# Optimization experiments

Hardware: AMD Instinct MI355X
Metric: run time of the kernel (lower is better)

## Reference

```python
import jax, jax.numpy as jnp
import numpy as np

N_HEAD = 16
LN_EPS = 1e-5     # torch LayerNorm default
ATTN_EPS = 1e-6   # fast-transformers CausalLinearAttention eps


def layer_norm(x, g, b):
    mu = x.mean(-1, keepdims=True)
    var = ((x - mu) ** 2).mean(-1, keepdims=True)
    return (x - mu) * jax.lax.rsqrt(var + LN_EPS) * g + b


def favor(x, omega):
    # Favor/Performer softmax-kernel features.
    # x: [B,S,H,dh], omega: [dh, m/2] -> phi: [B,S,H,m] with m = 2*(dh//2) = dh
    dh = x.shape[-1]
    m = 2 * omega.shape[-1]
    xs = x * (dh ** -0.25)  # x * sqrt(softmax_temp), softmax_temp = 1/sqrt(dh)
    u = jnp.einsum('bshd,dm->bshm', xs, omega)
    h = 0.5 * jnp.sum(xs * xs, axis=-1, keepdims=True)  # ||x||^2 / 2
    return jnp.concatenate([jnp.exp(u - h), jnp.exp(-u - h)], axis=-1) * (m ** -0.5)


def causal_linear_attention(q, k, v):
    # q,k: [B,S,H,M] feature-mapped; v: [B,S,H,Dv]
    # out[i] = (phiQ_i @ sum_{j<=i} phiK_j v_j^T) / (phiQ_i . sum_{j<=i} phiK_j)
    B, S, H, M = q.shape
    Dv = v.shape[-1]
    qT = jnp.moveaxis(q, 1, 0)  # [S,B,H,M]
    kT = jnp.moveaxis(k, 1, 0)
    vT = jnp.moveaxis(v, 1, 0)  # [S,B,H,Dv]
    S0 = jnp.zeros((B, H, M, Dv), q.dtype)
    z0 = jnp.zeros((B, H, M), q.dtype)

    def step(carry, qkv):
        Sst, zst = carry
        qi, ki, vi = qkv
        Sst = Sst + ki[..., :, None] * vi[..., None, :]  # [B,H,M,Dv]
        zst = zst + ki                                   # [B,H,M]
        num = jnp.einsum('bhm,bhmd->bhd', qi, Sst)
        den = jnp.einsum('bhm,bhm->bh', qi, zst) + ATTN_EPS
        return (Sst, zst), num / den[..., None]

    _, out = jax.lax.scan(step, (S0, z0), (qT, kT, vT))
    return jnp.moveaxis(out, 0, 1)  # [B,S,H,Dv]


def forward(x, Wq, bq, Wk, bk, Wv, bv, Wo, bo, omega,
            ln1_g, ln1_b, ln2_g, ln2_b, W1, bf1, W2, bf2):
    L = Wq.shape[0]
    B, S, D = x.shape
    dh = D // N_HEAD
    out = x
    for l in range(L):  # fixed small layer count
        q = (out @ Wq[l] + bq[l]).reshape(B, S, N_HEAD, dh)
        k = (out @ Wk[l] + bk[l]).reshape(B, S, N_HEAD, dh)
        v = (out @ Wv[l] + bv[l]).reshape(B, S, N_HEAD, dh)
        Qf = favor(q, omega[l])
        Kf = favor(k, omega[l])
        a = causal_linear_attention(Qf, Kf, v).reshape(B, S, D)
        a = a @ Wo[l] + bo[l]
        h = layer_norm(out + a, ln1_g[l], ln1_b[l])          # norm1 (post-norm)
        y = jax.nn.relu(h @ W1[l] + bf1[l]) @ W2[l] + bf2[l]  # FFN
        out = layer_norm(h + y, ln2_g[l], ln2_b[l])          # norm2
    return out


def setup_inputs() -> dict:
    key = jax.random.key(0)
    L, B, S, D, DFF = 3, 2, 1024, 1024, 4096
    dh = D // N_HEAD
    ks = jax.random.split(key, 8)
    g = lambda k, shape: jax.random.normal(k, shape, jnp.float32) * 0.02
    return {
        'x': jax.random.normal(ks[0], (B, S, D), jnp.float32),
        'Wq': g(ks[1], (L, D, D)), 'bq': jnp.zeros((L, D), jnp.float32),
        'Wk': g(ks[2], (L, D, D)), 'bk': jnp.zeros((L, D), jnp.float32),
        'Wv': g(ks[3], (L, D, D)), 'bv': jnp.zeros((L, D), jnp.float32),
        'Wo': g(ks[4], (L, D, D)), 'bo': jnp.zeros((L, D), jnp.float32),
        'omega': jax.random.normal(ks[5], (L, dh, dh // 2), jnp.float32),
        'ln1_g': jnp.ones((L, D), jnp.float32), 'ln1_b': jnp.zeros((L, D), jnp.float32),
        'ln2_g': jnp.ones((L, D), jnp.float32), 'ln2_b': jnp.zeros((L, D), jnp.float32),
        'W1': g(ks[6], (L, D, DFF)), 'bf1': jnp.zeros((L, DFF), jnp.float32),
        'W2': g(ks[7], (L, DFF, D)), 'bf2': jnp.zeros((L, D), jnp.float32),
    }


def reference(x, Wq, bq, Wk, bk, Wv, bv, Wo, bo, omega,
              ln1_g, ln1_b, ln2_g, ln2_b, W1, bf1, W2, bf2):
    return forward(x, Wq, bq, Wk, bk, Wv, bv, Wo, bo, omega,
                   ln1_g, ln1_b, ln2_g, ln2_b, W1, bf1, W2, bf2)
```

## Files before the change

### kernel.cpp

```cpp
#include <hip/hip_runtime.h>

typedef unsigned int u32;
typedef unsigned short u16;
typedef unsigned long long u64;

#define LN_EPS 1e-5f
#define ATTN_EPS 1e-6f

typedef __bf16 bf16x8 __attribute__((ext_vector_type(8)));
typedef short shortx8 __attribute__((ext_vector_type(8)));
typedef float fx4 __attribute__((ext_vector_type(4)));
typedef float fx16 __attribute__((ext_vector_type(16)));

__device__ __forceinline__ u16 f2bf(float f){
  union{float f; u32 u;} x; x.f = f;
  u32 r = 0x7fffu + ((x.u>>16)&1u);
  return (u16)((x.u + r)>>16);
}
__device__ __forceinline__ float bf2f(u16 u){
  union{u32 u; float f;} x; x.u = ((u32)u)<<16; return x.f;
}
__device__ __forceinline__ bf16x8 ldfrag(const u16* p){
  return __builtin_bit_cast(bf16x8, *(const shortx8*)p);
}

__device__ __forceinline__ void async16(const void* g, void* l){
  typedef const __attribute__((address_space(1))) void gas_t;
  typedef __attribute__((address_space(3))) void las_t;
  __builtin_amdgcn_global_load_lds((gas_t*)(u64)g, (las_t*)(u32)(u64)l, 16, 0, 0);
}

__global__ void detect_kernel(const u16* __restrict__ ln1g, int* __restrict__ flag){
  if (threadIdx.x == 0 && blockIdx.x == 0)
    *flag = (ln1g[0] == 0x3F80u) ? 1 : 0;
}

__global__ __launch_bounds__(256) void cvt_small(
    const void* p0, const void* p1, const void* p2, const void* p3,
    const void* p4, const void* p5, const void* p6, const void* p7,
    const void* p8, const void* p9, const void* p10,
    float* __restrict__ out, const int* __restrict__ flagp)
{
  int i = blockIdx.x*256 + threadIdx.x;
  if (i >= 46080) return;
  const void* src; int off;
  if      (i < 3072)  { src=p0;  off=i; }
  else if (i < 6144)  { src=p1;  off=i-3072; }
  else if (i < 9216)  { src=p2;  off=i-6144; }
  else if (i < 12288) { src=p3;  off=i-9216; }
  else if (i < 18432) { src=p4;  off=i-12288; }
  else if (i < 21504) { src=p5;  off=i-18432; }
  else if (i < 24576) { src=p6;  off=i-21504; }
  else if (i < 27648) { src=p7;  off=i-24576; }
  else if (i < 30720) { src=p8;  off=i-27648; }
  else if (i < 43008) { src=p9;  off=i-30720; }
  else                { src=p10; off=i-43008; }
  float v;
  if (*flagp){ union{u32 u; float f;} x; x.u = ((u32)((const u16*)src)[off])<<16; v = x.f; }
  else v = ((const float*)src)[off];
  out[i] = v;
}

__global__ __launch_bounds__(256) void cvt_x(const void* __restrict__ in, float* __restrict__ out,
                                             u16* __restrict__ outbf, int n, const int* __restrict__ flagp){
  int i = blockIdx.x*256 + threadIdx.x;
  if (i >= n) return;
  float v;
  if (*flagp){ union{u32 u; float f;} x; x.u = ((u32)((const u16*)in)[i])<<16; v = x.f; }
  else v = ((const float*)in)[i];
  out[i] = v;
  outbf[i] = f2bf(v);
}

__global__ __launch_bounds__(256) void transpose_cvtL(
    const void* __restrict__ W, u16* __restrict__ Wt,
    int K, int N, size_t zsrc, size_t zdst, const int* __restrict__ flagp)
{
  __shared__ float s[32][33];
  const size_t eoff = (size_t)blockIdx.z * zsrc;
  Wt += (size_t)blockIdx.z * zdst;
  const int bx = blockIdx.x, by = blockIdx.y;
  const int tid = threadIdx.x;
  const int c = tid & 31, r = tid >> 5;
  const int isbf = *flagp;
#pragma unroll
  for (int i = 0; i < 4; ++i){
    int k = by*32 + r + i*8, n = bx*32 + c;
    size_t idx = eoff + (size_t)k*N + n;
    float v;
    if (isbf){ union{u32 u; float f;} x; x.u = ((u32)((const u16*)W)[idx])<<16; v = x.f; }
    else v = ((const float*)W)[idx];
    s[r + i*8][c] = v;
  }
  __syncthreads();
#pragma unroll
  for (int i = 0; i < 4; ++i){
    int n = bx*32 + r + i*8, k = by*32 + c;
    Wt[(size_t)n*K + k] = f2bf(s[c][r + i*8]);
  }
}

__global__ __launch_bounds__(256) void transpose_cvtQ(
    const void* __restrict__ W0, const void* __restrict__ W1,
    const void* __restrict__ W2, const void* __restrict__ W3,
    u16* __restrict__ Wt, const int* __restrict__ flagp)
{
  __shared__ float s[32][33];
  const int z = blockIdx.z, l = z >> 2, m = z & 3;
  const void* W = (m==0)?W0:((m==1)?W1:((m==2)?W2:W3));
  const size_t eoff = (size_t)l * 1048576;
  Wt += (size_t)z * 1048576;
  const int bx = blockIdx.x, by = blockIdx.y;
  const int tid = threadIdx.x;
  const int c = tid & 31, r = tid >> 5;
  const int isbf = *flagp;
#pragma unroll
  for (int i = 0; i < 4; ++i){
    int k = by*32 + r + i*8, n = bx*32 + c;
    size_t idx = eoff + (size_t)k*1024 + n;
    float v;
    if (isbf){ union{u32 u; float f;} x; x.u = ((u32)((const u16*)W)[idx])<<16; v = x.f; }
    else v = ((const float*)W)[idx];
    s[r + i*8][c] = v;
  }
  __syncthreads();
#pragma unroll
  for (int i = 0; i < 4; ++i){
    int n = bx*32 + r + i*8, k = by*32 + c;
    Wt[(size_t)n*1024 + k] = f2bf(s[c][r + i*8]);
  }
}

__global__ __launch_bounds__(512, 2) void mfma_gemm8(
    const u16* __restrict__ A, const u16* __restrict__ W,
    const float* __restrict__ bias,
    float* __restrict__ C, u16* __restrict__ Cbf,
    int N, int Kst, int kstep_z, int klen,
    size_t wz, size_t cz, int bz, int bias_all, int relu)
{
  __shared__ u16 As[3][256*64];
  __shared__ u16 Bs[3][128*64];
  const int z = blockIdx.z;
  W    += (size_t)z * wz;
  bias += (size_t)z * bz;
  if (C) C += (size_t)z * cz;
  const int kbeg = z * kstep_z;
  const int tid = threadIdx.x;
  const int lane = tid & 63, wid = tid >> 6;
  const size_t KstS = (size_t)Kst;

  int bx = blockIdx.x, by = blockIdx.y;
  {
    const int gx = gridDim.x, gy = gridDim.y;
    if (((gx & 3) == 0) && ((gy & 1) == 0)) {
      const int cw = gx >> 2, ch = gy >> 1;
      if (((cw & (cw-1)) == 0) && ((ch & (ch-1)) == 0)) {
        const int o = by*gx + bx;
        const int xcd = o & 7, k = o >> 3;
        const int lgw = 31 - __clz(cw);
        bx = (xcd & 3)*cw + (k & (cw-1));
        by = (xcd >> 2)*ch + (k >> lgw);
      }
    }
  }
  const int row0 = by * 256, col0 = bx * 128;

  const int sR = tid >> 3;
  const int sC = ((tid & 7) ^ (sR & 7)) << 3;
  const u16* gAr = A + (size_t)(row0 + sR)*KstS + kbeg + sC;
  const u16* gBr = W + (size_t)(col0 + sR)*KstS + kbeg + sC;

#define STAGE_H0(b, ks) { const size_t ko = (size_t)(ks) << 6; \
    async16(gAr + ko,                &As[b][tid*8]); \
    async16(gAr + 64*KstS + ko,      &As[b][4096 + tid*8]); \
    async16(gBr + ko,                &Bs[b][tid*8]); }
#define STAGE_H1(b, ks) { const size_t ko = (size_t)(ks) << 6; \
    async16(gAr + 128*KstS + ko,     &As[b][8192 + tid*8]); \
    async16(gAr + 192*KstS + ko,     &As[b][12288 + tid*8]); \
    async16(gBr + 64*KstS + ko,      &Bs[b][4096 + tid*8]); }

  const int nt = klen >> 6;
  STAGE_H0(0, 0) STAGE_H1(0, 0)
  STAGE_H0(1, 1) STAGE_H1(1, 1)
  __builtin_amdgcn_s_waitcnt(0x0F76);
  __builtin_amdgcn_s_barrier();

  const int l31 = lane & 31, hi = lane >> 5;
  const int wr = (wid >> 1) * 64;
  const int wc = (wid & 1) * 64;
  fx16 acc[2][2] = {};

  for (int t = 0; t < nt; ++t){
    const int buf = t % 3;
    const int nx   = (t + 2 < nt) ? (t + 2) : (nt - 1);
    const int nbuf = (t + 2) % 3;

    bf16x8 a0[2][2], b0[2][2];
#pragma unroll
    for (int kk = 0; kk < 2; ++kk){
      const int sl = ((2*kk + hi) ^ (l31 & 7)) << 3;
#pragma unroll
      for (int mt = 0; mt < 2; ++mt)
        a0[mt][kk] = ldfrag(&As[buf][(wr + mt*32 + l31)*64 + sl]);
#pragma unroll
      for (int ntc = 0; ntc < 2; ++ntc)
        b0[ntc][kk] = ldfrag(&Bs[buf][(wc + ntc*32 + l31)*64 + sl]);
    }
    STAGE_H0(nbuf, nx)
    __builtin_amdgcn_s_barrier();
    __builtin_amdgcn_s_setprio(1);
#pragma unroll
    for (int kk = 0; kk < 2; ++kk)
#pragma unroll
      for (int mt = 0; mt < 2; ++mt)
#pragma unroll
        for (int ntc = 0; ntc < 2; ++ntc)
          acc[mt][ntc] = __builtin_amdgcn_mfma_f32_32x32x16_bf16(a0[mt][kk], b0[ntc][kk], acc[mt][ntc], 0,0,0);
    __builtin_amdgcn_s_setprio(0);
    __builtin_amdgcn_s_barrier();

    bf16x8 a1[2][2], b1[2][2];
#pragma unroll
    for (int kk = 0; kk < 2; ++kk){
      const int sl = ((2*(kk+2) + hi) ^ (l31 & 7)) << 3;
#pragma unroll
      for (int mt = 0; mt < 2; ++mt)
        a1[mt][kk] = ldfrag(&As[buf][(wr + mt*32 + l31)*64 + sl]);
#pragma unroll
      for (int ntc = 0; ntc < 2; ++ntc)
        b1[ntc][kk] = ldfrag(&Bs[buf][(wc + ntc*32 + l31)*64 + sl]);
    }
    STAGE_H1(nbuf, nx)
    __builtin_amdgcn_s_waitcnt(0x0F76);
    __builtin_amdgcn_s_barrier();
    __builtin_amdgcn_s_setprio(1);
#pragma unroll
    for (int kk = 0; kk < 2; ++kk)
#pragma unroll
      for (int mt = 0; mt < 2; ++mt)
#pragma unroll
        for (int ntc = 0; ntc < 2; ++ntc)
          acc[mt][ntc] = __builtin_amdgcn_mfma_f32_32x32x16_bf16(a1[mt][kk], b1[ntc][kk], acc[mt][ntc], 0,0,0);
    __builtin_amdgcn_s_setprio(0);
    __builtin_amdgcn_s_barrier();
  }
  __builtin_amdgcn_s_waitcnt(0x0F70);

  const int rbase = 4*hi;
#pragma unroll
  for (int ntc = 0; ntc < 2; ++ntc){
    const int col = col0 + wc + ntc*32 + l31;
    const float bv = (bias_all || z == 0) ? bias[col] : 0.f;
#pragma unroll
    for (int mt = 0; mt < 2; ++mt){
#pragma unroll
      for (int r = 0; r < 16; ++r){
        const int row = row0 + wr + mt*32 + rbase + (r & 3) + 8*(r >> 2);
        float v = acc[mt][ntc][r] + bv;
        if (relu) v = fmaxf(v, 0.f);
        if (C)   C[(size_t)row*N + col] = v;
        if (Cbf) Cbf[(size_t)row*N + col] = f2bf(v);
      }
    }
  }
#undef STAGE_H0
#undef STAGE_H1
}

__global__ __launch_bounds__(256) void chunk_kv_favor(
    const float* __restrict__ Kraw, const float* __restrict__ V,
    const float* __restrict__ omega,
    float* __restrict__ KV, float* __restrict__ Ksum, u16* __restrict__ Kb)
{
  __shared__ float Xs[64][68];
  __shared__ float Vs[64][64];
  __shared__ float Ph[64][68];
  __shared__ float Om[64][32];
  const int blk = blockIdx.x;
  const int c = blk & 15, h = (blk >> 4) & 15, b = blk >> 8;
  const int tid = threadIdx.x;
  const int t0 = b*1024 + c*64;

  for (int i = tid; i < 2048; i += 256)
    Om[i>>5][i&31] = omega[i];
  for (int i = tid; i < 1024; i += 256){
    int j = i >> 4, m4 = (i & 15) << 2;
    size_t src = (size_t)(t0 + j)*1024 + h*64 + m4;
    float4 kv4 = *(const float4*)&Kraw[src];
    float4 xs4 = make_float4(kv4.x*0.35355339059327373f, kv4.y*0.35355339059327373f,
                             kv4.z*0.35355339059327373f, kv4.w*0.35355339059327373f);
    *(float4*)&Xs[j][m4] = xs4;
    *(float4*)&Vs[j][m4] = *(const float4*)&V[src];
  }
  __syncthreads();

  {
    const int tok = tid >> 2, q = tid & 3;
    float u[8] = {0,0,0,0,0,0,0,0};
    float hh = 0.f;
    for (int d = 0; d < 64; ++d){
      float xv = Xs[tok][d];
      hh = fmaf(xv, xv, hh);
      float4 o0 = *(const float4*)&Om[d][q*8];
      float4 o1 = *(const float4*)&Om[d][q*8+4];
      u[0]=fmaf(xv,o0.x,u[0]); u[1]=fmaf(xv,o0.y,u[1]);
      u[2]=fmaf(xv,o0.z,u[2]); u[3]=fmaf(xv,o0.w,u[3]);
      u[4]=fmaf(xv,o1.x,u[4]); u[5]=fmaf(xv,o1.y,u[5]);
      u[6]=fmaf(xv,o1.z,u[6]); u[7]=fmaf(xv,o1.w,u[7]);
    }
    hh *= 0.5f;
#pragma unroll
    for (int i = 0; i < 8; ++i){
      Ph[tok][q*8+i]    = expf( u[i] - hh) * 0.125f;
      Ph[tok][32+q*8+i] = expf(-u[i] - hh) * 0.125f;
    }
  }
  __syncthreads();

  {
    const int r = tid >> 2, c4 = (tid & 3) << 4;
    u16 tmp[16];
#pragma unroll
    for (int j = 0; j < 16; ++j) tmp[j] = f2bf(Ph[r][c4 + j]);
    size_t g = (size_t)(t0 + r)*1024 + h*64 + c4;
    *(uint4*)(Kb + g)     = *(uint4*)&tmp[0];
    *(uint4*)(Kb + g + 8) = *(uint4*)&tmp[8];
  }

  const int m = tid & 63, dg = tid >> 6;
  float acc[16] = {0.f};
  for (int j = 0; j < 64; ++j){
    float kv = Ph[j][m];
#pragma unroll
    for (int di = 0; di < 16; ++di)
      acc[di] = fmaf(Vs[j][dg*16+di], kv, acc[di]);
  }
  size_t outb = (size_t)blk * 4096;
#pragma unroll
  for (int di = 0; di < 16; ++di)
    KV[outb + (size_t)(dg*16+di)*64 + m] = acc[di];
  if (tid < 64){
    float s = 0.f;
    for (int j = 0; j < 64; ++j) s += Ph[j][tid];
    Ksum[(size_t)blk*64 + tid] = s;
  }
}

__global__ __launch_bounds__(256) void chunk_scan(float* __restrict__ KV, float* __restrict__ Ksum)
{
  int blk = blockIdx.x;
  int bh = blk >> 4, ec = blk & 15;
  int e = ec*256 + threadIdx.x;
  size_t base = (size_t)bh * 65536 + e;
  float run = 0.f;
  for (int c = 0; c < 16; ++c){
    size_t idx = base + (size_t)c*4096;
    float t = KV[idx]; KV[idx] = run; run += t;
  }
  if (ec == 0 && threadIdx.x < 64){
    size_t kb = (size_t)bh * 1024 + threadIdx.x;
    float rz = 0.f;
    for (int c = 0; c < 16; ++c){
      size_t idx = kb + c*64;
      float t = Ksum[idx]; Ksum[idx] = rz; rz += t;
    }
  }
}

__global__ __launch_bounds__(256) void attn_kernel(
    const float* __restrict__ Qraw, const u16* __restrict__ Kbf,
    const float* __restrict__ V, const float* __restrict__ KVt,
    const float* __restrict__ Ksum, const float* __restrict__ omega,
    u16* __restrict__ Outbf)
{
  __shared__ u16 Qs[64][72];
  __shared__ u16 Ks[64][72];
  __shared__ u16 Ss[64][72];
  __shared__ u16 Vt[64][72];
  __shared__ u16 Pt[64][72];
  __shared__ float Vrow[64][68];
  __shared__ float Om[64][32];
  __shared__ float densum[64];

  const int blk = blockIdx.x;
  const int c = blk & 15, h = (blk >> 4) & 15, b = blk >> 8;
  const int tid = threadIdx.x;
  const int lane = tid & 63, w = tid >> 6;
  const int quad = lane >> 4, l16 = lane & 15;
  const int t0 = b*1024 + c*64;
  const int r = tid >> 2, q4 = (tid & 3) << 4;
  const size_t g = (size_t)(t0 + r)*1024 + h*64 + q4;

  for (int i = tid; i < 2048; i += 256)
    Om[i>>5][i&31] = omega[i];
  {
    *(uint4*)&Ks[r][q4]   = *(const uint4*)(Kbf + g);
    *(uint4*)&Ks[r][q4+8] = *(const uint4*)(Kbf + g + 8);
    const float* vg = V + g;
    *(float4*)&Vrow[r][q4+0]  = *(const float4*)(vg+0);
    *(float4*)&Vrow[r][q4+4]  = *(const float4*)(vg+4);
    *(float4*)&Vrow[r][q4+8]  = *(const float4*)(vg+8);
    *(float4*)&Vrow[r][q4+12] = *(const float4*)(vg+12);
    const float* pg = KVt + (size_t)blk*4096 + r*64 + q4;
    u16 tmp[16];
#pragma unroll
    for (int j = 0; j < 16; ++j) tmp[j] = f2bf(pg[j]);
    *(uint4*)&Pt[r][q4]   = *(uint4*)&tmp[0];
    *(uint4*)&Pt[r][q4+8] = *(uint4*)&tmp[8];
  }
  __syncthreads();
  {
    const int d = tid >> 2, j16 = (tid & 3) << 4;
    u16 tmp[16];
#pragma unroll
    for (int j = 0; j < 16; ++j) tmp[j] = f2bf(Vrow[j16+j][d]);
    *(uint4*)&Vt[d][j16]   = *(uint4*)&tmp[0];
    *(uint4*)&Vt[d][j16+8] = *(uint4*)&tmp[8];
  }
  __syncthreads();
  {
    const float* qg = Qraw + g;
    float4 a0 = *(const float4*)(qg+0), a1 = *(const float4*)(qg+4);
    float4 a2 = *(const float4*)(qg+8), a3 = *(const float4*)(qg+12);
    const float sc = 0.35355339059327373f;
    *(float4*)&Vrow[r][q4+0]  = make_float4(a0.x*sc, a0.y*sc, a0.z*sc, a0.w*sc);
    *(float4*)&Vrow[r][q4+4]  = make_float4(a1.x*sc, a1.y*sc, a1.z*sc, a1.w*sc);
    *(float4*)&Vrow[r][q4+8]  = make_float4(a2.x*sc, a2.y*sc, a2.z*sc, a2.w*sc);
    *(float4*)&Vrow[r][q4+12] = make_float4(a3.x*sc, a3.y*sc, a3.z*sc, a3.w*sc);
  }
  __syncthreads();
  {
    const int tok = tid >> 2, q = tid & 3;
    float u[8] = {0,0,0,0,0,0,0,0};
    float hh = 0.f;
    for (int d = 0; d < 64; ++d){
      float xv = Vrow[tok][d];
      hh = fmaf(xv, xv, hh);
      float4 o0 = *(const float4*)&Om[d][q*8];
      float4 o1 = *(const float4*)&Om[d][q*8+4];
      u[0]=fmaf(xv,o0.x,u[0]); u[1]=fmaf(xv,o0.y,u[1]);
      u[2]=fmaf(xv,o0.z,u[2]); u[3]=fmaf(xv,o0.w,u[3]);
      u[4]=fmaf(xv,o1.x,u[4]); u[5]=fmaf(xv,o1.y,u[5]);
      u[6]=fmaf(xv,o1.z,u[6]); u[7]=fmaf(xv,o1.w,u[7]);
    }
    hh *= 0.5f;
#pragma unroll
    for (int i = 0; i < 8; i += 2){
      float e0 = expf( u[i]   - hh) * 0.125f;
      float e1 = expf( u[i+1] - hh) * 0.125f;
      *(u32*)&Qs[tok][q*8+i]    = (u32)f2bf(e0) | ((u32)f2bf(e1) << 16);
      float f0 = expf(-u[i]   - hh) * 0.125f;
      float f1 = expf(-u[i+1] - hh) * 0.125f;
      *(u32*)&Qs[tok][32+q*8+i] = (u32)f2bf(f0) | ((u32)f2bf(f1) << 16);
    }
  }
  __syncthreads();

  const int iw0 = w*16;
  bf16x8 aq0 = ldfrag(&Qs[iw0+l16][quad*8]);
  bf16x8 aq1 = ldfrag(&Qs[iw0+l16][32+quad*8]);
  fx4 sacc[4];
#pragma unroll
  for (int u = 0; u < 4; ++u){
    sacc[u] = (fx4){0.f,0.f,0.f,0.f};
    bf16x8 b0 = ldfrag(&Ks[u*16+l16][quad*8]);
    bf16x8 b1 = ldfrag(&Ks[u*16+l16][32+quad*8]);
    sacc[u] = __builtin_amdgcn_mfma_f32_16x16x32_bf16(aq0, b0, sacc[u], 0, 0, 0);
    sacc[u] = __builtin_amdgcn_mfma_f32_16x16x32_bf16(aq1, b1, sacc[u], 0, 0, 0);
  }
  float rs[4] = {0.f,0.f,0.f,0.f};
#pragma unroll
  for (int u = 0; u < 4; ++u){
    const int jl = u*16 + l16;
#pragma unroll
    for (int rr = 0; rr < 4; ++rr){
      const int il = iw0 + quad*4 + rr;
      float v = (jl <= il) ? sacc[u][rr] : 0.f;
      rs[rr] += v;
      Ss[il][jl] = f2bf(v);
    }
  }
#pragma unroll
  for (int off = 1; off < 16; off <<= 1){
#pragma unroll
    for (int rr = 0; rr < 4; ++rr) rs[rr] += __shfl_xor(rs[rr], off);
  }
  if (l16 == 0){
#pragma unroll
    for (int rr = 0; rr < 4; ++rr) densum[iw0 + quad*4 + rr] = rs[rr];
  }
  __syncthreads();

  {
    const int row = iw0 + l16;
    const float* zp = Ksum + (size_t)blk*64;
    float dp = 0.f;
#pragma unroll
    for (int m = 0; m < 16; ++m){
      const int mm = quad*16 + m;
      dp = fmaf(bf2f(Qs[row][mm]), zp[mm], dp);
    }
    dp += __shfl_xor(dp, 16);
    dp += __shfl_xor(dp, 32);
    if (quad == 0) densum[row] = densum[row] + dp + ATTN_EPS;
  }
  __syncthreads();

  bf16x8 as0 = ldfrag(&Ss[iw0+l16][quad*8]);
  bf16x8 as1 = ldfrag(&Ss[iw0+l16][32+quad*8]);
  fx4 oacc[4];
#pragma unroll
  for (int u = 0; u < 4; ++u){
    const int d0 = u*16;
    oacc[u] = (fx4){0.f,0.f,0.f,0.f};
    oacc[u] = __builtin_amdgcn_mfma_f32_16x16x32_bf16(as0, ldfrag(&Vt[d0+l16][quad*8]),    oacc[u], 0,0,0);
    oacc[u] = __builtin_amdgcn_mfma_f32_16x16x32_bf16(as1, ldfrag(&Vt[d0+l16][32+quad*8]), oacc[u], 0,0,0);
    oacc[u] = __builtin_amdgcn_mfma_f32_16x16x32_bf16(aq0, ldfrag(&Pt[d0+l16][quad*8]),    oacc[u], 0,0,0);
    oacc[u] = __builtin_amdgcn_mfma_f32_16x16x32_bf16(aq1, ldfrag(&Pt[d0+l16][32+quad*8]), oacc[u], 0,0,0);
  }
#pragma unroll
  for (int u = 0; u < 4; ++u){
    const int d = u*16 + l16;
#pragma unroll
    for (int rr = 0; rr < 4; ++rr){
      const int il = iw0 + quad*4 + rr;
      const float o = oacc[u][rr] / densum[il];
      Outbf[(size_t)(t0 + il)*1024 + h*64 + d] = f2bf(o);
    }
  }
}

__global__ __launch_bounds__(256) void resid_ln(
    const float* __restrict__ X, const float* __restrict__ Y0, const float* __restrict__ Y1,
    const float* __restrict__ Y2, const float* __restrict__ Y3,
    const float* __restrict__ g, const float* __restrict__ b,
    float* __restrict__ Dst, u16* __restrict__ DstBf,
    void* __restrict__ OutPtr, const int* __restrict__ flagp)
{
  __shared__ float rs[4], rss[4];
  int row = blockIdx.x, tid = threadIdx.x;
  int lane = tid & 63, wv = tid >> 6;
  size_t base = (size_t)row * 1024;
  int c = tid << 2;
  float4 xv = *(const float4*)&X[base + c];
  float4 y0 = *(const float4*)&Y0[base + c];
  float4 y1 = *(const float4*)&Y1[base + c];
  float v0 = xv.x+y0.x+y1.x, v1 = xv.y+y0.y+y1.y, v2 = xv.z+y0.z+y1.z, v3 = xv.w+y0.w+y1.w;
  if (Y2){
    float4 y2 = *(const float4*)&Y2[base + c];
    float4 y3 = *(const float4*)&Y3[base + c];
    v0 += y2.x + y3.x; v1 += y2.y + y3.y; v2 += y2.z + y3.z; v3 += y2.w + y3.w;
  }
  float s = v0+v1+v2+v3;
  float ss = v0*v0+v1*v1+v2*v2+v3*v3;
  for (int off = 32; off; off >>= 1){
    s  += __shfl_down(s, off);
    ss += __shfl_down(ss, off);
  }
  if (lane == 0){ rs[wv] = s; rss[wv] = ss; }
  __syncthreads();
  float S  = rs[0]+rs[1]+rs[2]+rs[3];
  float SS = rss[0]+rss[1]+rss[2]+rss[3];
  float mu = S * (1.f/1024.f);
  float var = SS * (1.f/1024.f) - mu*mu;
  float rinv = rsqrtf(var + LN_EPS);
  float4 gv = *(const float4*)(g + c);
  float4 bb = *(const float4*)(b + c);
  float o0 = (v0-mu)*rinv*gv.x + bb.x;
  float o1 = (v1-mu)*rinv*gv.y + bb.y;
  float o2 = (v2-mu)*rinv*gv.z + bb.z;
  float o3 = (v3-mu)*rinv*gv.w + bb.w;
  *(float4*)&Dst[base + c] = make_float4(o0,o1,o2,o3);
  uint2 ob;
  ob.x = (u32)f2bf(o0) | ((u32)f2bf(o1) << 16);
  ob.y = (u32)f2bf(o2) | ((u32)f2bf(o3) << 16);
  *(uint2*)(DstBf + base + c) = ob;
  if (OutPtr){
    if (*flagp){
      *(uint2*)((u16*)OutPtr + base + c) = ob;
    } else {
      *(float4*)((float*)OutPtr + base + c) = make_float4(o0,o1,o2,o3);
    }
  }
}

extern "C" void kernel_launch(void* const* d_in, const int* in_sizes, int n_in,
                              void* d_out, int out_size, void* d_ws, size_t ws_size,
                              hipStream_t stream)
{
  (void)in_sizes; (void)n_in; (void)out_size; (void)ws_size;

  float* ws   = (float*)d_ws;
  float* R    = ws;
  float* P0   = R  + 2097152;
  float* P1   = P0 + 2097152;
  float* P2   = P1 + 2097152;
  float* P3   = P2 + 2097152;
  float* KVb  = P3 + 2097152;
  float* Ks   = KVb + 2097152;
  float* smallP = Ks + 32768;
  float* pend = smallP + 46080;
  int* flag = (int*)pend;
  u16* abf  = (u16*)(pend + 4);
  u16* hbf  = abf  + 2097152;
  u16* t1bf = hbf  + 2097152;
  u16* fbf  = t1bf + 2097152;
  u16* kpbf = fbf  + 8388608;
  u16* WtQ  = kpbf + 2097152;
  u16* WtF1 = WtQ  + 12582912;
  u16* WtF2 = WtF1 + 12582912;

  float* bqF  = smallP + 0;
  float* boF  = smallP + 9216;
  float* omF  = smallP + 12288;
  float* l1gF = smallP + 18432;
  float* l1bF = smallP + 21504;
  float* l2gF = smallP + 24576;
  float* l2bF = smallP + 27648;
  float* bf1F = smallP + 30720;
  float* bf2F = smallP + 43008;

  detect_kernel<<<1, 64, 0, stream>>>((const u16*)d_in[10], flag);
  cvt_small<<<180, 256, 0, stream>>>(d_in[2], d_in[4], d_in[6], d_in[8], d_in[9],
                                     d_in[10], d_in[11], d_in[12], d_in[13],
                                     d_in[15], d_in[17], smallP, flag);
  cvt_x<<<8192, 256, 0, stream>>>(d_in[0], R, abf, 2097152, flag);

  transpose_cvtQ<<<dim3(32, 32, 12), 256, 0, stream>>>(d_in[1], d_in[3], d_in[5], d_in[7],
                                                       WtQ, flag);
  transpose_cvtL<<<dim3(128, 32, 3), 256, 0, stream>>>(d_in[14], WtF1, 1024, 4096,
                                                       4194304, 4194304, flag);
  transpose_cvtL<<<dim3(32, 128, 3), 256, 0, stream>>>(d_in[16], WtF2, 4096, 1024,
                                                       4194304, 4194304, flag);

  dim3 gQKV(8, 8, 3);
  dim3 gO(8, 8, 2);
  dim3 gF1(32, 8, 1);
  dim3 gF2(8, 8, 4);

  for (int l = 0; l < 3; ++l){
    const size_t wQ = (size_t)l * 4194304;

    mfma_gemm8<<<gQKV, 512, 0, stream>>>(abf, WtQ + wQ, bqF + l*1024, P0, (u16*)nullptr,
                                         1024, 1024, 0, 1024,
                                         1048576, 2097152, 3072, 1, 0);
    chunk_kv_favor<<<512, 256, 0, stream>>>(P1, P2, omF + l*2048, KVb, Ks, kpbf);
    chunk_scan<<<512, 256, 0, stream>>>(KVb, Ks);
    attn_kernel<<<512, 256, 0, stream>>>(P0, kpbf, P2, KVb, Ks, omF + l*2048, t1bf);

    mfma_gemm8<<<gO, 512, 0, stream>>>(t1bf, WtQ + wQ + 3145728, boF + l*1024, P0, (u16*)nullptr,
                                       1024, 1024, 512, 512,
                                       0, 2097152, 0, 0, 0);
    resid_ln<<<2048, 256, 0, stream>>>(R, P0, P1, nullptr, nullptr,
                                       l1gF + l*1024, l1bF + l*1024,
                                       KVb, hbf, nullptr, flag);

    mfma_gemm8<<<gF1, 512, 0, stream>>>(hbf, WtF1 + wQ, bf1F + l*4096, (float*)nullptr, fbf,
                                        4096, 1024, 0, 1024,
                                        0, 0, 0, 1, 1);

    mfma_gemm8<<<gF2, 512, 0, stream>>>(fbf, WtF2 + wQ, bf2F + l*1024, P0, (u16*)nullptr,
                                        1024, 4096, 1024, 1024,
                                        0, 2097152, 0, 0, 0);

    resid_ln<<<2048, 256, 0, stream>>>(KVb, P0, P1, P2, P3,
                                       l2gF + l*1024, l2bF + l*1024,
                                       R, abf, (l == 2) ? d_out : nullptr, flag);
  }
}
```

Before: 678.7 us.

## Merge half-stage GEMM pipeline into single stage and split O-proj K four ways

The GEMM main loop now loads all four k-slices of fragments at once, issues the whole next-stage prefetch in one go, and runs all MFMAs with a single barrier per iteration instead of two half-stages with three barriers. This cuts synchronization overhead but holds more fragment registers live, which may lower occupancy or reduce how well LDS reads overlap with loads. Separately, the output-projection GEMM uses a 4-way split-K of 256 instead of 2-way of 512 to launch more blocks, and the following residual-LayerNorm kernel now reads the extra partial buffers P2 and P3.

```diff
diff --git a/kernel.cpp b/kernel.cpp
--- a/kernel.cpp
+++ b/kernel.cpp
@@ -170,18 +170,17 @@
   const u16* gAr = A + (size_t)(row0 + sR)*KstS + kbeg + sC;
   const u16* gBr = W + (size_t)(col0 + sR)*KstS + kbeg + sC;
 
-#define STAGE_H0(b, ks) { const size_t ko = (size_t)(ks) << 6; \
+#define STAGE_ALL(b, ks) { const size_t ko = (size_t)(ks) << 6; \
     async16(gAr + ko,                &As[b][tid*8]); \
     async16(gAr + 64*KstS + ko,      &As[b][4096 + tid*8]); \
-    async16(gBr + ko,                &Bs[b][tid*8]); }
-#define STAGE_H1(b, ks) { const size_t ko = (size_t)(ks) << 6; \
     async16(gAr + 128*KstS + ko,     &As[b][8192 + tid*8]); \
     async16(gAr + 192*KstS + ko,     &As[b][12288 + tid*8]); \
+    async16(gBr + ko,                &Bs[b][tid*8]); \
     async16(gBr + 64*KstS + ko,      &Bs[b][4096 + tid*8]); }
 
   const int nt = klen >> 6;
-  STAGE_H0(0, 0) STAGE_H1(0, 0)
-  STAGE_H0(1, 1) STAGE_H1(1, 1)
+  STAGE_ALL(0, 0)
+  STAGE_ALL(1, 1)
   __builtin_amdgcn_s_waitcnt(0x0F76);
   __builtin_amdgcn_s_barrier();
 
@@ -195,53 +194,28 @@
     const int nx   = (t + 2 < nt) ? (t + 2) : (nt - 1);
     const int nbuf = (t + 2) % 3;
 
-    bf16x8 a0[2][2], b0[2][2];
-#pragma unroll
-    for (int kk = 0; kk < 2; ++kk){
-      const int sl = ((2*kk + hi) ^ (l31 & 7)) << 3;
+    bf16x8 af[4][2], bg[4][2];
+#pragma unroll
+    for (int kh = 0; kh < 4; ++kh){
+      const int sl = ((2*kh + hi) ^ (l31 & 7)) << 3;
 #pragma unroll
       for (int mt = 0; mt < 2; ++mt)
-        a0[mt][kk] = ldfrag(&As[buf][(wr + mt*32 + l31)*64 + sl]);
+        af[kh][mt] = ldfrag(&As[buf][(wr + mt*32 + l31)*64 + sl]);
 #pragma unroll
       for (int ntc = 0; ntc < 2; ++ntc)
-        b0[ntc][kk] = ldfrag(&Bs[buf][(wc + ntc*32 + l31)*64 + sl]);
-    }
-    STAGE_H0(nbuf, nx)
-    __builtin_amdgcn_s_barrier();
+        bg[kh][ntc] = ldfrag(&Bs[buf][(wc + ntc*32 + l31)*64 + sl]);
+    }
+    STAGE_ALL(nbuf, nx)
     __builtin_amdgcn_s_setprio(1);
 #pragma unroll
-    for (int kk = 0; kk < 2; ++kk)
+    for (int kh = 0; kh < 4; ++kh)
 #pragma unroll
       for (int mt = 0; mt < 2; ++mt)
 #pragma unroll
         for (int ntc = 0; ntc < 2; ++ntc)
-          acc[mt][ntc] = __builtin_amdgcn_mfma_f32_32x32x16_bf16(a0[mt][kk], b0[ntc][kk], acc[mt][ntc], 0,0,0);
+          acc[mt][ntc] = __builtin_amdgcn_mfma_f32_32x32x16_bf16(af[kh][mt], bg[kh][ntc], acc[mt][ntc], 0,0,0);
     __builtin_amdgcn_s_setprio(0);
-    __builtin_amdgcn_s_barrier();
-
-    bf16x8 a1[2][2], b1[2][2];
-#pragma unroll
-    for (int kk = 0; kk < 2; ++kk){
-      const int sl = ((2*(kk+2) + hi) ^ (l31 & 7)) << 3;
-#pragma unroll
-      for (int mt = 0; mt < 2; ++mt)
-        a1[mt][kk] = ldfrag(&As[buf][(wr + mt*32 + l31)*64 + sl]);
-#pragma unroll
-      for (int ntc = 0; ntc < 2; ++ntc)
-        b1[ntc][kk] = ldfrag(&Bs[buf][(wc + ntc*32 + l31)*64 + sl]);
-    }
-    STAGE_H1(nbuf, nx)
     __builtin_amdgcn_s_waitcnt(0x0F76);
-    __builtin_amdgcn_s_barrier();
-    __builtin_amdgcn_s_setprio(1);
-#pragma unroll
-    for (int kk = 0; kk < 2; ++kk)
-#pragma unroll
-      for (int mt = 0; mt < 2; ++mt)
-#pragma unroll
-        for (int ntc = 0; ntc < 2; ++ntc)
-          acc[mt][ntc] = __builtin_amdgcn_mfma_f32_32x32x16_bf16(a1[mt][kk], b1[ntc][kk], acc[mt][ntc], 0,0,0);
-    __builtin_amdgcn_s_setprio(0);
     __builtin_amdgcn_s_barrier();
   }
   __builtin_amdgcn_s_waitcnt(0x0F70);
@@ -263,8 +237,7 @@
       }
     }
   }
-#undef STAGE_H0
-#undef STAGE_H1
+#undef STAGE_ALL
 }
 
 __global__ __launch_bounds__(256) void chunk_kv_favor(
@@ -634,7 +607,7 @@
                                                        4194304, 4194304, flag);
 
   dim3 gQKV(8, 8, 3);
-  dim3 gO(8, 8, 2);
+  dim3 gO(8, 8, 4);
   dim3 gF1(32, 8, 1);
   dim3 gF2(8, 8, 4);
 
@@ -649,9 +622,9 @@
     attn_kernel<<<512, 256, 0, stream>>>(P0, kpbf, P2, KVb, Ks, omF + l*2048, t1bf);
 
     mfma_gemm8<<<gO, 512, 0, stream>>>(t1bf, WtQ + wQ + 3145728, boF + l*1024, P0, (u16*)nullptr,
-                                       1024, 1024, 512, 512,
+                                       1024, 1024, 256, 256,
                                        0, 2097152, 0, 0, 0);
-    resid_ln<<<2048, 256, 0, stream>>>(R, P0, P1, nullptr, nullptr,
+    resid_ln<<<2048, 256, 0, stream>>>(R, P0, P1, P2, P3,
                                        l1gF + l*1024, l1bF + l*1024,
                                        KVb, hbf, nullptr, flag);
 
```

After: 669.0 us. Within noise of the previous version (-1.4%).
